# Optimization experiments

Measured on AMD Instinct MI355X. Metric: run time of the kernel, lower is better.

The kernel has to match this reference:

```python
import jax, jax.numpy as jnp
import numpy as np

LATENT = 256; INPUT = 128; NUNITS = 256; DEC_OUT = 128
NTRAJ = 256; NTP = 512
INTERP = 2  # hard-coded in the original forward

def _mlp_sig(x, w1, b1, w2, b2):
    return jax.nn.sigmoid(jnp.tanh(x @ w1 + b1) @ w2 + b2)

def _mlp_lin(x, w1, b1, w2, b2):
    return jnp.tanh(x @ w1 + b1) @ w2 + b2

def _gru_step(y, yt, x, ug, ugt, rg, ns):
    # x: [N, 2*INPUT]; first half = features, second half = observation mask channels
    xh = x[:, :INPUT]
    yc = jnp.concatenate([y, xh], axis=-1)                 # [N, LATENT+INPUT]
    u = _mlp_sig(yc, *ug)
    ut = _mlp_sig(yc, *ugt)
    r = _mlp_sig(yc, *rg)
    new_state = _mlp_lin(jnp.concatenate([y * r, xh], axis=-1), *ns)
    new_y = (1.0 - u) * new_state + u * y
    new_yt = (1.0 - ut) * new_state + ut * yt
    mask = (jnp.sum(x[:, INPUT:], axis=-1, keepdims=True) > 0).astype(x.dtype)
    return mask * new_y + (1.0 - mask) * y, mask * new_yt + (1.0 - mask) * yt

def setup_inputs():
    key = jax.random.key(0)
    ks = iter(jax.random.split(key, 32))
    def p(shape):
        return jax.random.normal(next(ks), shape, dtype=jnp.float32) * 0.05
    d = {}
    d["data"] = jax.random.normal(next(ks), (NTRAJ, NTP, 2 * INPUT), dtype=jnp.float32)
    dts = jax.random.uniform(next(ks), (NTRAJ, NTP), dtype=jnp.float32) + 0.1
    d["time_steps"] = jnp.cumsum(dts, axis=1)              # strictly increasing times
    gin = LATENT + INPUT
    for name in ("ug", "ugt", "rg", "rgt", "ns"):
        d[name + "_w1"] = p((gin, NUNITS)); d[name + "_b1"] = jnp.zeros((NUNITS,), jnp.float32)
        d[name + "_w2"] = p((NUNITS, LATENT)); d[name + "_b2"] = jnp.zeros((LATENT,), jnp.float32)
    d["dk_w1"] = p((LATENT, LATENT)); d["dk_b1"] = jnp.zeros((LATENT,), jnp.float32)
    d["dk_w2"] = p((LATENT, 1)); d["dk_b2"] = jnp.zeros((1,), jnp.float32)
    d["dec_w"] = p((LATENT, DEC_OUT)); d["dec_b"] = jnp.zeros((DEC_OUT,), jnp.float32)
    return d

def reference(data, time_steps,
              ug_w1, ug_b1, ug_w2, ug_b2,
              ugt_w1, ugt_b1, ugt_w2, ugt_b2,
              rg_w1, rg_b1, rg_w2, rg_b2,
              rgt_w1, rgt_b1, rgt_w2, rgt_b2,
              ns_w1, ns_b1, ns_w2, ns_b2,
              dk_w1, dk_b1, dk_w2, dk_b2,
              dec_w, dec_b):
    # Note: reset_gate_target (rgt_*) is computed but never used in the original forward.
    ug = (ug_w1, ug_b1, ug_w2, ug_b2)
    ugt = (ugt_w1, ugt_b1, ugt_w2, ugt_b2)
    rg = (rg_w1, rg_b1, rg_w2, rg_b2)
    ns = (ns_w1, ns_b1, ns_w2, ns_b2)
    n_traj = data.shape[0]
    lin = jnp.linspace(0.0, 1.0, INTERP + 1, dtype=data.dtype)  # [3]
    y0 = jnp.zeros((n_traj, LATENT), data.dtype)
    # step i=0: no decay interpolation, yi_decay = prev_y (zeros)
    y, yt = _gru_step(y0, y0, data[:, 0, :], ug, ugt, rg, ns)
    dts = time_steps[:, 1:] - time_steps[:, :-1]                # [N, T-1]
    xs = jnp.moveaxis(data[:, 1:, :], 1, 0)                     # [T-1, N, 2I]

    def step(carry, inp):
        y, yt = carry
        x, dt = inp
        decay = jax.nn.relu(jax.nn.relu(y @ dk_w1 + dk_b1) @ dk_w2 + dk_b2)  # [N,1]
        e = jnp.exp(-decay * (dt[:, None] * lin[None, :]))                   # [N,3]
        ydec = yt[:, None, :] + (y - yt)[:, None, :] * e[:, :, None]         # [N,3,L]
        vol = jnp.mean(ydec[:, :-1, :] @ dec_w + dec_b, axis=-2)             # [N,D]
        y2, yt2 = _gru_step(ydec[:, -1, :], yt, x, ug, ugt, rg, ns)
        return (y2, yt2), vol

    (y, yt), vols = jax.lax.scan(step, (y, yt), (xs, dts.T))
    prev_y = y[None, :, :]                       # [1, N, L]
    volume_dt = jnp.transpose(vols, (1, 0, 2))   # [N, T-1, D]
    return prev_y, volume_dt, dts
```

## Files before the change

kernel.cpp:

```cpp
#include <hip/hip_runtime.h>
#include <hip/hip_fp16.h>

#define NTRAJ   256
#define NTP     512
#define NSTEPS  511
#define LATENT  256
#define INPUT   128
#define DEC_OUT 128

#define OUT_VOL ((size_t)NTRAJ * LATENT)
#define OUT_DTS (OUT_VOL + (size_t)NTRAJ * NSTEPS * DEC_OUT)

#define WU_UG1  0
#define WU_UG2  49152
#define WU_UGT1 81920
#define WU_UGT2 131072
#define WU_RG1  163840
#define WU_RG2  212992
#define WU_NS1  245760
#define WU_NS2  294912
#define WU_DK1  327680
#define WU_DEC  360448
#define WU_TOT  376832

typedef _Float16 h2_t __attribute__((ext_vector_type(2)));
union U32H2 { unsigned int u; h2_t h; };

__device__ __forceinline__ float dot2f(unsigned int wu, unsigned int xu, float acc) {
#if defined(__has_builtin) && __has_builtin(__builtin_amdgcn_fdot2)
    U32H2 a, b; a.u = wu; b.u = xu;
    return __builtin_amdgcn_fdot2(a.h, b.h, acc, false);
#else
    U32H2 a, b; a.u = wu; b.u = xu;
    return acc + (float)a.h.x * (float)b.h.x + (float)a.h.y * (float)b.h.y;
#endif
}

__device__ __forceinline__ float wred(float v) {
    #pragma unroll
    for (int off = 32; off; off >>= 1) v += __shfl_down(v, off, 64);
    return v;
}
__device__ __forceinline__ float fast_sigmoid(float x) { return 1.0f / (1.0f + __expf(-x)); }
__device__ __forceinline__ float fast_tanh(float x) {
    float e = __expf(2.0f * x);
    return 1.0f - 2.0f / (e + 1.0f);
}
__device__ __forceinline__ unsigned int packpair(float v) {
    float vn = __shfl_xor(v, 1, 64);
    U32H2 r; r.h.x = (_Float16)v; r.h.y = (_Float16)vn;
    return r.u;
}

extern "C" __global__ void __launch_bounds__(256)
convert_w(const float* __restrict__ ug_w1, const float* __restrict__ ug_w2,
          const float* __restrict__ ugt_w1, const float* __restrict__ ugt_w2,
          const float* __restrict__ rg_w1, const float* __restrict__ rg_w2,
          const float* __restrict__ ns_w1, const float* __restrict__ ns_w2,
          const float* __restrict__ dk_w1, const float* __restrict__ dec_w,
          unsigned int* __restrict__ ws)
{
    const int i = blockIdx.x * 256 + threadIdx.x;
    const float* s; int o; int cbits;
    if      (i < WU_UG2)  { s = ug_w1;  o = i;           cbits = 8; }
    else if (i < WU_UGT1) { s = ug_w2;  o = i - WU_UG2;  cbits = 8; }
    else if (i < WU_UGT2) { s = ugt_w1; o = i - WU_UGT1; cbits = 8; }
    else if (i < WU_RG1)  { s = ugt_w2; o = i - WU_UGT2; cbits = 8; }
    else if (i < WU_RG2)  { s = rg_w1;  o = i - WU_RG1;  cbits = 8; }
    else if (i < WU_NS1)  { s = rg_w2;  o = i - WU_RG2;  cbits = 8; }
    else if (i < WU_NS2)  { s = ns_w1;  o = i - WU_NS1;  cbits = 8; }
    else if (i < WU_DK1)  { s = ns_w2;  o = i - WU_NS2;  cbits = 8; }
    else if (i < WU_DEC)  { s = dk_w1;  o = i - WU_DK1;  cbits = 8; }
    else                  { s = dec_w;  o = i - WU_DEC;  cbits = 7; }
    const int C  = 1 << cbits;
    const int kp = o >> cbits;
    const int c  = o & (C - 1);
    const float v0 = s[(2 * kp) * C + c];
    const float v1 = s[(2 * kp + 1) * C + c];
    const unsigned int h0 = __half_as_ushort(__float2half(v0));
    const unsigned int h1 = __half_as_ushort(__float2half(v1));
    ws[i] = h0 | (h1 << 16);
}

extern "C" __global__ void __launch_bounds__(512, 2)
rnn_decay_kernel3(const float* __restrict__ data, const float* __restrict__ ts,
                  const float* __restrict__ ug_b1, const float* __restrict__ ug_b2,
                  const float* __restrict__ ugt_b1, const float* __restrict__ ugt_b2,
                  const float* __restrict__ rg_b1, const float* __restrict__ rg_b2,
                  const float* __restrict__ ns_b1, const float* __restrict__ ns_b2,
                  const float* __restrict__ dk_b1, const float* __restrict__ dk_w2,
                  const float* __restrict__ dk_b2, const float* __restrict__ dec_b,
                  const unsigned int* __restrict__ wsu, float* __restrict__ out)
{
    __shared__ __align__(16) float s_part[8192];
    __shared__ unsigned int s_in_h[192];
    __shared__ unsigned int s_ns_h[192];
    __shared__ unsigned int s_y_h[128];
    __shared__ unsigned int s_a_h[128];
    __shared__ unsigned int s_b_h[128];
    __shared__ unsigned int s_c_h[128];
    __shared__ unsigned int s_v_h[128];
    __shared__ float s_ut[256];
    __shared__ float s_red[8];

    const int tid  = threadIdx.x;
    const int w    = tid >> 6;
    const int lane = tid & 63;
    const int c    = tid & 255;
    const int cl4  = lane << 2;
    const int traj = blockIdx.x;

    const unsigned int* UG1  = wsu + WU_UG1;  const unsigned int* UG2  = wsu + WU_UG2;
    const unsigned int* UGT1 = wsu + WU_UGT1; const unsigned int* UGT2 = wsu + WU_UGT2;
    const unsigned int* RG1  = wsu + WU_RG1;  const unsigned int* RG2  = wsu + WU_RG2;
    const unsigned int* NS1  = wsu + WU_NS1;  const unsigned int* NS2  = wsu + WU_NS2;
    const unsigned int* DK1  = wsu + WU_DK1;  const unsigned int* DECW = wsu + WU_DEC;

    const float* dbase = data + (size_t)traj * NTP * (2 * INPUT);
    const float* tbase = ts + (size_t)traj * NTP;
    float* vol_out = out + OUT_VOL + (size_t)traj * NSTEPS * DEC_OUT;
    float* dts_out = out + OUT_DTS + (size_t)traj * NSTEPS;

    if (tid < 256)
        for (int t = c; t < NSTEPS; t += 256)
            dts_out[t] = tbase[t + 1] - tbase[t];

    float r_y = 0.f, r_yt = 0.f;

    for (int t = -1; t < NSTEPS; ++t) {
        const bool first = (t < 0);

        if (tid < 256) {
            const float xv = first ? dbase[c] : dbase[(size_t)(t + 1) * 256 + c];
            float mv = (c >= 128) ? xv : 0.f;
            mv = wred(mv);
            if (lane == 0) s_red[w] = mv;
            if (c < 128) {
                const unsigned int px = packpair(xv);
                if (!(lane & 1)) { s_in_h[128 + (c >> 1)] = px; s_ns_h[128 + (c >> 1)] = px; }
            }
            if (first && !(lane & 1)) s_in_h[c >> 1] = 0u;
        }

        float r_ydec = 0.f, r_u = 0.f, r_r = 0.f;
        bool maskv;

        if (!first) {
            float4 aD = make_float4(0, 0, 0, 0);
            const int kp0 = w << 4;
            #pragma unroll 4
            for (int i = 0; i < 16; ++i) {
                const unsigned int x = s_y_h[kp0 + i];
                const uint4 wv = *(const uint4*)(DK1 + (size_t)(kp0 + i) * 256 + cl4);
                aD.x = dot2f(wv.x, x, aD.x); aD.y = dot2f(wv.y, x, aD.y);
                aD.z = dot2f(wv.z, x, aD.z); aD.w = dot2f(wv.w, x, aD.w);
            }
            *(float4*)(s_part + (w << 8) + cl4) = aD;
            __syncthreads();
            if (tid < 256) {
                float v = dk_b1[c];
                #pragma unroll
                for (int i = 0; i < 8; ++i) v += s_part[(i << 8) + c];
                v = fmaxf(v, 0.f);
                float pv = wred(v * dk_w2[c]);
                if (lane == 0) s_red[4 + w] = pv;
            }
            __syncthreads();
            const float decay = fmaxf(s_red[4] + s_red[5] + s_red[6] + s_red[7] + dk_b2[0], 0.f);
            maskv = (s_red[0] + s_red[1] + s_red[2] + s_red[3]) > 0.f;
            if (tid < 256) {
                const float dt = tbase[t + 1] - tbase[t];
                const float diff = r_y - r_yt;
                const float ef = __expf(-decay * dt);
                const float eh = __expf(-0.5f * decay * dt);
                r_ydec = r_yt + diff * ef;
                const float vol = 0.5f * (r_y + r_yt + diff * eh);
                const unsigned int pd = packpair(r_ydec);
                const unsigned int pvv = packpair(vol);
                if (!(lane & 1)) { s_in_h[c >> 1] = pd; s_v_h[c >> 1] = pvv; }
            }
            __syncthreads();
        } else {
            __syncthreads();
            maskv = (s_red[0] + s_red[1] + s_red[2] + s_red[3]) > 0.f;
        }

        if (!first) {
            float4 aE = make_float4(0, 0, 0, 0);
            const int hh = lane >> 5, cl = (lane & 31) << 2;
            const int kpb = (w << 4) + hh;
            #pragma unroll 4
            for (int i = 0; i < 8; ++i) {
                const int kp = kpb + (i << 1);
                const uint4 wv = *(const uint4*)(DECW + (size_t)kp * 128 + cl);
                const unsigned int x = s_v_h[kp];
                aE.x = dot2f(wv.x, x, aE.x); aE.y = dot2f(wv.y, x, aE.y);
                aE.z = dot2f(wv.z, x, aE.z); aE.w = dot2f(wv.w, x, aE.w);
            }
            *(float4*)(s_part + 6144 + ((w << 1) + hh) * 128 + cl) = aE;
        }
        {
            float4 aA = make_float4(0, 0, 0, 0), aB = aA, aC = aA;
            const int kp0 = w * 24;
            #pragma unroll 4
            for (int i = 0; i < 24; ++i) {
                const int kp = kp0 + i;
                const unsigned int x = s_in_h[kp];
                const uint4 wa = *(const uint4*)(UG1  + (size_t)kp * 256 + cl4);
                const uint4 wb = *(const uint4*)(UGT1 + (size_t)kp * 256 + cl4);
                const uint4 wc = *(const uint4*)(RG1  + (size_t)kp * 256 + cl4);
                aA.x = dot2f(wa.x, x, aA.x); aA.y = dot2f(wa.y, x, aA.y);
                aA.z = dot2f(wa.z, x, aA.z); aA.w = dot2f(wa.w, x, aA.w);
                aB.x = dot2f(wb.x, x, aB.x); aB.y = dot2f(wb.y, x, aB.y);
                aB.z = dot2f(wb.z, x, aB.z); aB.w = dot2f(wb.w, x, aB.w);
                aC.x = dot2f(wc.x, x, aC.x); aC.y = dot2f(wc.y, x, aC.y);
                aC.z = dot2f(wc.z, x, aC.z); aC.w = dot2f(wc.w, x, aC.w);
            }
            *(float4*)(s_part + (w << 8) + cl4)          = aA;
            *(float4*)(s_part + 2048 + (w << 8) + cl4)   = aB;
            *(float4*)(s_part + 4096 + (w << 8) + cl4)   = aC;
        }
        __syncthreads();
        {
            const int s = tid >> 8;
            float v = (s ? ugt_b1 : ug_b1)[c];
            const float* pb = s_part + (s ? 2048 : 0) + c;
            #pragma unroll
            for (int i = 0; i < 8; ++i) v += pb[i << 8];
            v = fast_tanh(v);
            const unsigned int pk = packpair(v);
            if (!(lane & 1)) (s ? s_b_h : s_a_h)[c >> 1] = pk;
            if (tid < 256) {
                float v2 = rg_b1[c];
                const float* pb2 = s_part + 4096 + c;
                #pragma unroll
                for (int i = 0; i < 8; ++i) v2 += pb2[i << 8];
                v2 = fast_tanh(v2);
                const unsigned int pk2 = packpair(v2);
                if (!(lane & 1)) s_c_h[c >> 1] = pk2;
            }
            if (!first && tid < 128) {
                float vd = dec_b[tid];
                const float* pbd = s_part + 6144 + tid;
                #pragma unroll
                for (int i = 0; i < 16; ++i) vd += pbd[i << 7];
                vol_out[(size_t)t * DEC_OUT + tid] = vd;
            }
        }
        __syncthreads();

        {
            float4 aA = make_float4(0, 0, 0, 0), aB = aA, aC = aA;
            const int kp0 = w << 4;
            #pragma unroll 4
            for (int i = 0; i < 16; ++i) {
                const int kp = kp0 + i;
                const unsigned int xa = s_a_h[kp];
                const unsigned int xb = s_b_h[kp];
                const unsigned int xc = s_c_h[kp];
                const uint4 wa = *(const uint4*)(UG2  + (size_t)kp * 256 + cl4);
                const uint4 wb = *(const uint4*)(UGT2 + (size_t)kp * 256 + cl4);
                const uint4 wc = *(const uint4*)(RG2  + (size_t)kp * 256 + cl4);
                aA.x = dot2f(wa.x, xa, aA.x); aA.y = dot2f(wa.y, xa, aA.y);
                aA.z = dot2f(wa.z, xa, aA.z); aA.w = dot2f(wa.w, xa, aA.w);
                aB.x = dot2f(wb.x, xb, aB.x); aB.y = dot2f(wb.y, xb, aB.y);
                aB.z = dot2f(wb.z, xb, aB.z); aB.w = dot2f(wb.w, xb, aB.w);
                aC.x = dot2f(wc.x, xc, aC.x); aC.y = dot2f(wc.y, xc, aC.y);
                aC.z = dot2f(wc.z, xc, aC.z); aC.w = dot2f(wc.w, xc, aC.w);
            }
            *(float4*)(s_part + (w << 8) + cl4)          = aA;
            *(float4*)(s_part + 2048 + (w << 8) + cl4)   = aB;
            *(float4*)(s_part + 4096 + (w << 8) + cl4)   = aC;
        }
        __syncthreads();
        {
            const int s = tid >> 8;
            float v = (s ? ugt_b2 : ug_b2)[c];
            const float* pb = s_part + (s ? 2048 : 0) + c;
            #pragma unroll
            for (int i = 0; i < 8; ++i) v += pb[i << 8];
            v = fast_sigmoid(v);
            if (s) s_ut[c] = v; else r_u = v;
            if (tid < 256) {
                float v2 = rg_b2[c];
                const float* pb2 = s_part + 4096 + c;
                #pragma unroll
                for (int i = 0; i < 8; ++i) v2 += pb2[i << 8];
                r_r = fast_sigmoid(v2);
                const unsigned int pk = packpair(r_ydec * r_r);
                if (!(lane & 1)) s_ns_h[c >> 1] = pk;
            }
        }
        __syncthreads();

        {
            float4 aA = make_float4(0, 0, 0, 0);
            const int kp0 = w * 24;
            #pragma unroll 4
            for (int i = 0; i < 24; ++i) {
                const int kp = kp0 + i;
                const unsigned int x = s_ns_h[kp];
                const uint4 wa = *(const uint4*)(NS1 + (size_t)kp * 256 + cl4);
                aA.x = dot2f(wa.x, x, aA.x); aA.y = dot2f(wa.y, x, aA.y);
                aA.z = dot2f(wa.z, x, aA.z); aA.w = dot2f(wa.w, x, aA.w);
            }
            *(float4*)(s_part + (w << 8) + cl4) = aA;
        }
        __syncthreads();
        if (tid < 256) {
            float v = ns_b1[c];
            #pragma unroll
            for (int i = 0; i < 8; ++i) v += s_part[(i << 8) + c];
            v = fast_tanh(v);
            const unsigned int pk = packpair(v);
            if (!(lane & 1)) s_a_h[c >> 1] = pk;
        }
        __syncthreads();

        {
            float4 aA = make_float4(0, 0, 0, 0);
            const int kp0 = w << 4;
            #pragma unroll 4
            for (int i = 0; i < 16; ++i) {
                const int kp = kp0 + i;
                const unsigned int x = s_a_h[kp];
                const uint4 wa = *(const uint4*)(NS2 + (size_t)kp * 256 + cl4);
                aA.x = dot2f(wa.x, x, aA.x); aA.y = dot2f(wa.y, x, aA.y);
                aA.z = dot2f(wa.z, x, aA.z); aA.w = dot2f(wa.w, x, aA.w);
            }
            *(float4*)(s_part + (w << 8) + cl4) = aA;
        }
        __syncthreads();
        if (tid < 256) {
            float nsv = ns_b2[c];
            #pragma unroll
            for (int i = 0; i < 8; ++i) nsv += s_part[(i << 8) + c];
            const float u = r_u, ut = s_ut[c];
            const float ny  = (1.f - u)  * nsv + u  * r_ydec;
            const float nyt = (1.f - ut) * nsv + ut * r_yt;
            r_y  = maskv ? ny  : r_ydec;
            r_yt = maskv ? nyt : r_yt;
            const unsigned int pk = packpair(r_y);
            if (!(lane & 1)) s_y_h[c >> 1] = pk;
        }
        __syncthreads();
    }

    if (tid < 256)
        out[(size_t)traj * 256 + c] = r_y;
}

extern "C" void kernel_launch(void* const* d_in, const int* in_sizes, int n_in,
                              void* d_out, int out_size, void* d_ws, size_t ws_size,
                              hipStream_t stream) {
    const float* data   = (const float*)d_in[0];
    const float* ts     = (const float*)d_in[1];
    const float* ug_w1  = (const float*)d_in[2];
    const float* ug_b1  = (const float*)d_in[3];
    const float* ug_w2  = (const float*)d_in[4];
    const float* ug_b2  = (const float*)d_in[5];
    const float* ugt_w1 = (const float*)d_in[6];
    const float* ugt_b1 = (const float*)d_in[7];
    const float* ugt_w2 = (const float*)d_in[8];
    const float* ugt_b2 = (const float*)d_in[9];
    const float* rg_w1  = (const float*)d_in[10];
    const float* rg_b1  = (const float*)d_in[11];
    const float* rg_w2  = (const float*)d_in[12];
    const float* rg_b2  = (const float*)d_in[13];
    const float* ns_w1  = (const float*)d_in[18];
    const float* ns_b1  = (const float*)d_in[19];
    const float* ns_w2  = (const float*)d_in[20];
    const float* ns_b2  = (const float*)d_in[21];
    const float* dk_w1  = (const float*)d_in[22];
    const float* dk_b1  = (const float*)d_in[23];
    const float* dk_w2  = (const float*)d_in[24];
    const float* dk_b2  = (const float*)d_in[25];
    const float* dec_w  = (const float*)d_in[26];
    const float* dec_b  = (const float*)d_in[27];

    unsigned int* wsu = (unsigned int*)d_ws;

    convert_w<<<WU_TOT / 256, 256, 0, stream>>>(ug_w1, ug_w2, ugt_w1, ugt_w2,
                                                rg_w1, rg_w2, ns_w1, ns_w2,
                                                dk_w1, dec_w, wsu);

    rnn_decay_kernel3<<<NTRAJ, 512, 0, stream>>>(
        data, ts, ug_b1, ug_b2, ugt_b1, ugt_b2, rg_b1, rg_b2, ns_b1, ns_b2,
        dk_b1, dk_w2, dk_b2, dec_b, wsu, (float*)d_out);
}
```

Before: 7.585 ms.

## Software-pipeline weight loads across GEMV stages with register prefetch and lighter barriers

Restructures the per-step GEMV chain so the global weight loads for the next stage (DK1, gate layer 1/2, NS1, NS2) are issued before the barrier that precedes it. They are held in registers and double-buffered within the gate matmuls, so memory latency overlaps with reductions and activations. Shared-memory input vectors are read as uint4 vectors, biases are hoisted out of the time loop, and __syncthreads is replaced by a raw s_barrier with an lgkmcnt wait. The cost is much higher register pressure (dozens of uint4 prefetch registers) under launch_bounds(512,2), which risks spills. The custom barrier also no longer waits for outstanding global loads, which the explicit prefetching relies on.

```diff
diff --git a/kernel.cpp b/kernel.cpp
--- a/kernel.cpp
+++ b/kernel.cpp
@@ -50,6 +50,12 @@
     float vn = __shfl_xor(v, 1, 64);
     U32H2 r; r.h.x = (_Float16)v; r.h.y = (_Float16)vn;
     return r.u;
+}
+
+__device__ __forceinline__ void barx() {
+    asm volatile("s_waitcnt lgkmcnt(0)");
+    __builtin_amdgcn_s_barrier();
+    __builtin_amdgcn_sched_barrier(0);
 }
 
 extern "C" __global__ void __launch_bounds__(256)
@@ -82,6 +88,37 @@
     ws[i] = h0 | (h1 << 16);
 }
 
+#define DOT1(acc, wv, xv) { \
+    acc.x = dot2f((wv).x, (xv), acc.x); acc.y = dot2f((wv).y, (xv), acc.y); \
+    acc.z = dot2f((wv).z, (xv), acc.z); acc.w = dot2f((wv).w, (xv), acc.w); }
+
+#define G1_LOAD(A, B, C_, base) { \
+    _Pragma("unroll") \
+    for (int j = 0; j < 4; ++j) { const int kp = kp24 + (base) + j; \
+        A[j]  = *(const uint4*)(UG1  + (size_t)kp * 256 + cl4); \
+        B[j]  = *(const uint4*)(UGT1 + (size_t)kp * 256 + cl4); \
+        C_[j] = *(const uint4*)(RG1  + (size_t)kp * 256 + cl4); } }
+
+#define G1_DOT(A, B, C_, base) { \
+    _Pragma("unroll") \
+    for (int j = 0; j < 4; ++j) { const unsigned int xv_ = x1[(base) + j]; \
+        DOT1(aA, A[j], xv_); DOT1(aB, B[j], xv_); DOT1(aC, C_[j], xv_); } }
+
+#define G2_LOAD(A, B, C_, base) { \
+    _Pragma("unroll") \
+    for (int j = 0; j < 4; ++j) { const int kp = kp16 + (base) + j; \
+        A[j]  = *(const uint4*)(UG2  + (size_t)kp * 256 + cl4); \
+        B[j]  = *(const uint4*)(UGT2 + (size_t)kp * 256 + cl4); \
+        C_[j] = *(const uint4*)(RG2  + (size_t)kp * 256 + cl4); } }
+
+#define G2_DOT(A, B, C_, base) { \
+    _Pragma("unroll") \
+    for (int j = 0; j < 4; ++j) { \
+        const unsigned int va_ = xa[(base) + j]; \
+        const unsigned int vb_ = xb[(base) + j]; \
+        const unsigned int vc_ = xc[(base) + j]; \
+        DOT1(aA, A[j], va_); DOT1(aB, B[j], vb_); DOT1(aC, C_[j], vc_); } }
+
 extern "C" __global__ void __launch_bounds__(512, 2)
 rnn_decay_kernel3(const float* __restrict__ data, const float* __restrict__ ts,
                   const float* __restrict__ ug_b1, const float* __restrict__ ug_b2,
@@ -93,13 +130,13 @@
                   const unsigned int* __restrict__ wsu, float* __restrict__ out)
 {
     __shared__ __align__(16) float s_part[8192];
-    __shared__ unsigned int s_in_h[192];
-    __shared__ unsigned int s_ns_h[192];
-    __shared__ unsigned int s_y_h[128];
-    __shared__ unsigned int s_a_h[128];
-    __shared__ unsigned int s_b_h[128];
-    __shared__ unsigned int s_c_h[128];
-    __shared__ unsigned int s_v_h[128];
+    __shared__ __align__(16) unsigned int s_in_h[192];
+    __shared__ __align__(16) unsigned int s_ns_h[192];
+    __shared__ __align__(16) unsigned int s_y_h[128];
+    __shared__ __align__(16) unsigned int s_a_h[128];
+    __shared__ __align__(16) unsigned int s_b_h[128];
+    __shared__ __align__(16) unsigned int s_c_h[128];
+    __shared__ __align__(16) unsigned int s_v_h[128];
     __shared__ float s_ut[256];
     __shared__ float s_red[8];
 
@@ -122,21 +159,38 @@
     float* dts_out = out + OUT_DTS + (size_t)traj * NSTEPS;
 
     if (tid < 256)
-        for (int t = c; t < NSTEPS; t += 256)
-            dts_out[t] = tbase[t + 1] - tbase[t];
+        for (int t0 = c; t0 < NSTEPS; t0 += 256)
+            dts_out[t0] = tbase[t0 + 1] - tbase[t0];
+
+    const float b1sel = ((tid >> 8) ? ugt_b1 : ug_b1)[c];
+    const float b2sel = ((tid >> 8) ? ugt_b2 : ug_b2)[c];
+    const float rgb1  = rg_b1[c];
+    const float rgb2  = rg_b2[c];
+    const float nsb1  = ns_b1[c];
+    const float nsb2  = ns_b2[c];
+    const float dkb1  = dk_b1[c];
+    const float dkw2  = dk_w2[c];
+    const float dkb2  = dk_b2[0];
+    const float decb  = dec_b[tid & 127];
 
     float r_y = 0.f, r_yt = 0.f;
+    uint4 dkP[16];
+
+    const int kp24 = w * 24;
+    const int kp16 = w << 4;
 
     for (int t = -1; t < NSTEPS; ++t) {
         const bool first = (t < 0);
 
+        float dt_t = 0.f;
         if (tid < 256) {
-            const float xv = first ? dbase[c] : dbase[(size_t)(t + 1) * 256 + c];
-            float mv = (c >= 128) ? xv : 0.f;
+            const float xval = first ? dbase[c] : dbase[(size_t)(t + 1) * 256 + c];
+            if (!first) dt_t = tbase[t + 1] - tbase[t];
+            float mv = (c >= 128) ? xval : 0.f;
             mv = wred(mv);
             if (lane == 0) s_red[w] = mv;
             if (c < 128) {
-                const unsigned int px = packpair(xv);
+                const unsigned int px = packpair(xval);
                 if (!(lane & 1)) { s_in_h[128 + (c >> 1)] = px; s_ns_h[128 + (c >> 1)] = px; }
             }
             if (first && !(lane & 1)) s_in_h[c >> 1] = 0u;
@@ -145,85 +199,98 @@
         float r_ydec = 0.f, r_u = 0.f, r_r = 0.f;
         bool maskv;
 
+        uint4 g1a[4], g1b[4], g1c[4];
+        uint4 g2a[4], g2b[4], g2c[4];
+        uint4 nsP[24];
+        uint4 nsQ[16];
+
         if (!first) {
-            float4 aD = make_float4(0, 0, 0, 0);
-            const int kp0 = w << 4;
-            #pragma unroll 4
-            for (int i = 0; i < 16; ++i) {
-                const unsigned int x = s_y_h[kp0 + i];
-                const uint4 wv = *(const uint4*)(DK1 + (size_t)(kp0 + i) * 256 + cl4);
-                aD.x = dot2f(wv.x, x, aD.x); aD.y = dot2f(wv.y, x, aD.y);
-                aD.z = dot2f(wv.z, x, aD.z); aD.w = dot2f(wv.w, x, aD.w);
-            }
+            unsigned int yv[16];
+            {
+                const uint4* sy = (const uint4*)(s_y_h + kp16);
+                #pragma unroll
+                for (int j = 0; j < 4; ++j) {
+                    const uint4 q = sy[j];
+                    yv[4*j+0] = q.x; yv[4*j+1] = q.y; yv[4*j+2] = q.z; yv[4*j+3] = q.w;
+                }
+            }
+            float4 aD = make_float4(0.f, 0.f, 0.f, 0.f);
+            #pragma unroll
+            for (int j = 0; j < 16; ++j) DOT1(aD, dkP[j], yv[j]);
+
+            G1_LOAD(g1a, g1b, g1c, 0);
+
             *(float4*)(s_part + (w << 8) + cl4) = aD;
-            __syncthreads();
+            barx();
             if (tid < 256) {
-                float v = dk_b1[c];
+                float v = dkb1;
                 #pragma unroll
                 for (int i = 0; i < 8; ++i) v += s_part[(i << 8) + c];
                 v = fmaxf(v, 0.f);
-                float pv = wred(v * dk_w2[c]);
+                const float pv = wred(v * dkw2);
                 if (lane == 0) s_red[4 + w] = pv;
             }
-            __syncthreads();
-            const float decay = fmaxf(s_red[4] + s_red[5] + s_red[6] + s_red[7] + dk_b2[0], 0.f);
+            barx();
+            const float decay = fmaxf(s_red[4] + s_red[5] + s_red[6] + s_red[7] + dkb2, 0.f);
             maskv = (s_red[0] + s_red[1] + s_red[2] + s_red[3]) > 0.f;
             if (tid < 256) {
-                const float dt = tbase[t + 1] - tbase[t];
                 const float diff = r_y - r_yt;
-                const float ef = __expf(-decay * dt);
-                const float eh = __expf(-0.5f * decay * dt);
+                const float ef = __expf(-decay * dt_t);
+                const float eh = __expf(-0.5f * decay * dt_t);
                 r_ydec = r_yt + diff * ef;
                 const float vol = 0.5f * (r_y + r_yt + diff * eh);
-                const unsigned int pd = packpair(r_ydec);
+                const unsigned int pd  = packpair(r_ydec);
                 const unsigned int pvv = packpair(vol);
                 if (!(lane & 1)) { s_in_h[c >> 1] = pd; s_v_h[c >> 1] = pvv; }
             }
-            __syncthreads();
+            barx();
         } else {
-            __syncthreads();
+            G1_LOAD(g1a, g1b, g1c, 0);
+            barx();
             maskv = (s_red[0] + s_red[1] + s_red[2] + s_red[3]) > 0.f;
         }
 
         if (!first) {
-            float4 aE = make_float4(0, 0, 0, 0);
+            float4 aE = make_float4(0.f, 0.f, 0.f, 0.f);
             const int hh = lane >> 5, cl = (lane & 31) << 2;
-            const int kpb = (w << 4) + hh;
+            const int kpb = kp16 + hh;
             #pragma unroll 4
             for (int i = 0; i < 8; ++i) {
                 const int kp = kpb + (i << 1);
                 const uint4 wv = *(const uint4*)(DECW + (size_t)kp * 128 + cl);
-                const unsigned int x = s_v_h[kp];
-                aE.x = dot2f(wv.x, x, aE.x); aE.y = dot2f(wv.y, x, aE.y);
-                aE.z = dot2f(wv.z, x, aE.z); aE.w = dot2f(wv.w, x, aE.w);
+                const unsigned int xv_ = s_v_h[kp];
+                DOT1(aE, wv, xv_);
             }
             *(float4*)(s_part + 6144 + ((w << 1) + hh) * 128 + cl) = aE;
         }
-        {
-            float4 aA = make_float4(0, 0, 0, 0), aB = aA, aC = aA;
-            const int kp0 = w * 24;
-            #pragma unroll 4
-            for (int i = 0; i < 24; ++i) {
-                const int kp = kp0 + i;
-                const unsigned int x = s_in_h[kp];
-                const uint4 wa = *(const uint4*)(UG1  + (size_t)kp * 256 + cl4);
-                const uint4 wb = *(const uint4*)(UGT1 + (size_t)kp * 256 + cl4);
-                const uint4 wc = *(const uint4*)(RG1  + (size_t)kp * 256 + cl4);
-                aA.x = dot2f(wa.x, x, aA.x); aA.y = dot2f(wa.y, x, aA.y);
-                aA.z = dot2f(wa.z, x, aA.z); aA.w = dot2f(wa.w, x, aA.w);
-                aB.x = dot2f(wb.x, x, aB.x); aB.y = dot2f(wb.y, x, aB.y);
-                aB.z = dot2f(wb.z, x, aB.z); aB.w = dot2f(wb.w, x, aB.w);
-                aC.x = dot2f(wc.x, x, aC.x); aC.y = dot2f(wc.y, x, aC.y);
-                aC.z = dot2f(wc.z, x, aC.z); aC.w = dot2f(wc.w, x, aC.w);
-            }
+
+        {
+            unsigned int x1[24];
+            {
+                const uint4* sx = (const uint4*)(s_in_h + kp24);
+                #pragma unroll
+                for (int j = 0; j < 6; ++j) {
+                    const uint4 q = sx[j];
+                    x1[4*j+0] = q.x; x1[4*j+1] = q.y; x1[4*j+2] = q.z; x1[4*j+3] = q.w;
+                }
+            }
+            float4 aA = make_float4(0.f,0.f,0.f,0.f), aB = aA, aC = aA;
+            uint4 qa[4], qb[4], qc[4];
+            G1_LOAD(qa, qb, qc, 4);     G1_DOT(g1a, g1b, g1c, 0);
+            G1_LOAD(g1a, g1b, g1c, 8);  G1_DOT(qa, qb, qc, 4);
+            G1_LOAD(qa, qb, qc, 12);    G1_DOT(g1a, g1b, g1c, 8);
+            G1_LOAD(g1a, g1b, g1c, 16); G1_DOT(qa, qb, qc, 12);
+            G1_LOAD(qa, qb, qc, 20);    G1_DOT(g1a, g1b, g1c, 16);
+            G1_DOT(qa, qb, qc, 20);
+            G2_LOAD(g2a, g2b, g2c, 0);
             *(float4*)(s_part + (w << 8) + cl4)          = aA;
             *(float4*)(s_part + 2048 + (w << 8) + cl4)   = aB;
             *(float4*)(s_part + 4096 + (w << 8) + cl4)   = aC;
         }
-        __syncthreads();
+        barx();
         {
             const int s = tid >> 8;
-            float v = (s ? ugt_b1 : ug_b1)[c];
+            float v = b1sel;
             const float* pb = s_part + (s ? 2048 : 0) + c;
             #pragma unroll
             for (int i = 0; i < 8; ++i) v += pb[i << 8];
@@ -231,7 +298,7 @@
             const unsigned int pk = packpair(v);
             if (!(lane & 1)) (s ? s_b_h : s_a_h)[c >> 1] = pk;
             if (tid < 256) {
-                float v2 = rg_b1[c];
+                float v2 = rgb1;
                 const float* pb2 = s_part + 4096 + c;
                 #pragma unroll
                 for (int i = 0; i < 8; ++i) v2 += pb2[i << 8];
@@ -240,49 +307,52 @@
                 if (!(lane & 1)) s_c_h[c >> 1] = pk2;
             }
             if (!first && tid < 128) {
-                float vd = dec_b[tid];
+                float vd = decb;
                 const float* pbd = s_part + 6144 + tid;
                 #pragma unroll
                 for (int i = 0; i < 16; ++i) vd += pbd[i << 7];
                 vol_out[(size_t)t * DEC_OUT + tid] = vd;
             }
         }
-        __syncthreads();
-
-        {
-            float4 aA = make_float4(0, 0, 0, 0), aB = aA, aC = aA;
-            const int kp0 = w << 4;
-            #pragma unroll 4
-            for (int i = 0; i < 16; ++i) {
-                const int kp = kp0 + i;
-                const unsigned int xa = s_a_h[kp];
-                const unsigned int xb = s_b_h[kp];
-                const unsigned int xc = s_c_h[kp];
-                const uint4 wa = *(const uint4*)(UG2  + (size_t)kp * 256 + cl4);
-                const uint4 wb = *(const uint4*)(UGT2 + (size_t)kp * 256 + cl4);
-                const uint4 wc = *(const uint4*)(RG2  + (size_t)kp * 256 + cl4);
-                aA.x = dot2f(wa.x, xa, aA.x); aA.y = dot2f(wa.y, xa, aA.y);
-                aA.z = dot2f(wa.z, xa, aA.z); aA.w = dot2f(wa.w, xa, aA.w);
-                aB.x = dot2f(wb.x, xb, aB.x); aB.y = dot2f(wb.y, xb, aB.y);
-                aB.z = dot2f(wb.z, xb, aB.z); aB.w = dot2f(wb.w, xb, aB.w);
-                aC.x = dot2f(wc.x, xc, aC.x); aC.y = dot2f(wc.y, xc, aC.y);
-                aC.z = dot2f(wc.z, xc, aC.z); aC.w = dot2f(wc.w, xc, aC.w);
-            }
+        barx();
+
+        {
+            unsigned int xa[16], xb[16], xc[16];
+            {
+                const uint4* pa_ = (const uint4*)(s_a_h + kp16);
+                const uint4* pb_ = (const uint4*)(s_b_h + kp16);
+                const uint4* pc_ = (const uint4*)(s_c_h + kp16);
+                #pragma unroll
+                for (int j = 0; j < 4; ++j) {
+                    uint4 q = pa_[j]; xa[4*j+0]=q.x; xa[4*j+1]=q.y; xa[4*j+2]=q.z; xa[4*j+3]=q.w;
+                    q = pb_[j];       xb[4*j+0]=q.x; xb[4*j+1]=q.y; xb[4*j+2]=q.z; xb[4*j+3]=q.w;
+                    q = pc_[j];       xc[4*j+0]=q.x; xc[4*j+1]=q.y; xc[4*j+2]=q.z; xc[4*j+3]=q.w;
+                }
+            }
+            float4 aA = make_float4(0.f,0.f,0.f,0.f), aB = aA, aC = aA;
+            uint4 qa[4], qb[4], qc[4];
+            G2_LOAD(qa, qb, qc, 4);     G2_DOT(g2a, g2b, g2c, 0);
+            G2_LOAD(g2a, g2b, g2c, 8);  G2_DOT(qa, qb, qc, 4);
+            G2_LOAD(qa, qb, qc, 12);    G2_DOT(g2a, g2b, g2c, 8);
+            G2_DOT(qa, qb, qc, 12);
+            #pragma unroll
+            for (int j = 0; j < 24; ++j)
+                nsP[j] = *(const uint4*)(NS1 + (size_t)(kp24 + j) * 256 + cl4);
             *(float4*)(s_part + (w << 8) + cl4)          = aA;
             *(float4*)(s_part + 2048 + (w << 8) + cl4)   = aB;
             *(float4*)(s_part + 4096 + (w << 8) + cl4)   = aC;
         }
-        __syncthreads();
+        barx();
         {
             const int s = tid >> 8;
-            float v = (s ? ugt_b2 : ug_b2)[c];
+            float v = b2sel;
             const float* pb = s_part + (s ? 2048 : 0) + c;
             #pragma unroll
             for (int i = 0; i < 8; ++i) v += pb[i << 8];
             v = fast_sigmoid(v);
             if (s) s_ut[c] = v; else r_u = v;
             if (tid < 256) {
-                float v2 = rg_b2[c];
+                float v2 = rgb2;
                 const float* pb2 = s_part + 4096 + c;
                 #pragma unroll
                 for (int i = 0; i < 8; ++i) v2 += pb2[i << 8];
@@ -291,48 +361,58 @@
                 if (!(lane & 1)) s_ns_h[c >> 1] = pk;
             }
         }
-        __syncthreads();
-
-        {
-            float4 aA = make_float4(0, 0, 0, 0);
-            const int kp0 = w * 24;
-            #pragma unroll 4
-            for (int i = 0; i < 24; ++i) {
-                const int kp = kp0 + i;
-                const unsigned int x = s_ns_h[kp];
-                const uint4 wa = *(const uint4*)(NS1 + (size_t)kp * 256 + cl4);
-                aA.x = dot2f(wa.x, x, aA.x); aA.y = dot2f(wa.y, x, aA.y);
-                aA.z = dot2f(wa.z, x, aA.z); aA.w = dot2f(wa.w, x, aA.w);
-            }
+        barx();
+
+        {
+            unsigned int xn[24];
+            {
+                const uint4* sn = (const uint4*)(s_ns_h + kp24);
+                #pragma unroll
+                for (int j = 0; j < 6; ++j) {
+                    const uint4 q = sn[j];
+                    xn[4*j+0] = q.x; xn[4*j+1] = q.y; xn[4*j+2] = q.z; xn[4*j+3] = q.w;
+                }
+            }
+            float4 aA = make_float4(0.f,0.f,0.f,0.f);
+            #pragma unroll
+            for (int j = 0; j < 24; ++j) DOT1(aA, nsP[j], xn[j]);
+            #pragma unroll
+            for (int j = 0; j < 16; ++j)
+                nsQ[j] = *(const uint4*)(NS2 + (size_t)(kp16 + j) * 256 + cl4);
             *(float4*)(s_part + (w << 8) + cl4) = aA;
         }
-        __syncthreads();
+        barx();
         if (tid < 256) {
-            float v = ns_b1[c];
+            float v = nsb1;
             #pragma unroll
             for (int i = 0; i < 8; ++i) v += s_part[(i << 8) + c];
             v = fast_tanh(v);
             const unsigned int pk = packpair(v);
             if (!(lane & 1)) s_a_h[c >> 1] = pk;
         }
-        __syncthreads();
-
-        {
-            float4 aA = make_float4(0, 0, 0, 0);
-            const int kp0 = w << 4;
-            #pragma unroll 4
-            for (int i = 0; i < 16; ++i) {
-                const int kp = kp0 + i;
-                const unsigned int x = s_a_h[kp];
-                const uint4 wa = *(const uint4*)(NS2 + (size_t)kp * 256 + cl4);
-                aA.x = dot2f(wa.x, x, aA.x); aA.y = dot2f(wa.y, x, aA.y);
-                aA.z = dot2f(wa.z, x, aA.z); aA.w = dot2f(wa.w, x, aA.w);
-            }
+        barx();
+
+        {
+            unsigned int xs[16];
+            {
+                const uint4* sa = (const uint4*)(s_a_h + kp16);
+                #pragma unroll
+                for (int j = 0; j < 4; ++j) {
+                    const uint4 q = sa[j];
+                    xs[4*j+0] = q.x; xs[4*j+1] = q.y; xs[4*j+2] = q.z; xs[4*j+3] = q.w;
+                }
+            }
+            float4 aA = make_float4(0.f,0.f,0.f,0.f);
+            #pragma unroll
+            for (int j = 0; j < 16; ++j) DOT1(aA, nsQ[j], xs[j]);
+            #pragma unroll
+            for (int j = 0; j < 16; ++j)
+                dkP[j] = *(const uint4*)(DK1 + (size_t)(kp16 + j) * 256 + cl4);
             *(float4*)(s_part + (w << 8) + cl4) = aA;
         }
-        __syncthreads();
+        barx();
         if (tid < 256) {
-            float nsv = ns_b2[c];
+            float nsv = nsb2;
             #pragma unroll
             for (int i = 0; i < 8; ++i) nsv += s_part[(i << 8) + c];
             const float u = r_u, ut = s_ut[c];
@@ -343,7 +423,7 @@
             const unsigned int pk = packpair(r_y);
             if (!(lane & 1)) s_y_h[c >> 1] = pk;
         }
-        __syncthreads();
+        barx();
     }
 
     if (tid < 256)
```

Measured after the change: 26.28 ms. 246% more time.
